# Performance work log

Measured on AMD Instinct MI355X. Metric: run time of the kernel, lower is better.

Reference implementation:

```python
import jax, jax.numpy as jnp
import numpy as np

B, S, D, H = 1, 4096, 1024, 16
HD = D // H  # head_dim = 64
NEG = -1e9


def _rotate_half(x):
    x1, x2 = jnp.split(x, 2, axis=-1)
    return jnp.concatenate([-x2, x1], axis=-1)


def _apply_rope(x, cos, sin):
    # x: [b, s, h, hd]; cos/sin: [s, hd] -> broadcast over batch and heads
    c = cos[None, :, None, :]
    s = sin[None, :, None, :]
    return x * c + _rotate_half(x) * s


def setup_inputs() -> dict:
    key = jax.random.key(0)
    kx, kq, ko = jax.random.split(key, 3)
    x = jax.random.normal(kx, (B, S, D), dtype=jnp.float32)
    # causal additive mask (finite large-negative for safe grads)
    i = jnp.arange(S)
    attn_mask = jnp.where(i[None, :] > i[:, None], NEG, 0.0).astype(jnp.float32)[None, None]
    # standard RoPE tables
    inv_freq = 1.0 / (10000.0 ** (np.arange(0, HD, 2, dtype=np.float32) / HD))
    ang = np.arange(S, dtype=np.float32)[:, None] * inv_freq[None, :]  # [S, HD/2]
    ang = np.concatenate([ang, ang], axis=-1)  # [S, HD]
    rope_cos = jnp.asarray(np.cos(ang))
    rope_sin = jnp.asarray(np.sin(ang))
    W_qkv = jax.random.normal(kq, (D, 3 * D), dtype=jnp.float32) * (D ** -0.5)
    W_out = jax.random.normal(ko, (D, D), dtype=jnp.float32) * (D ** -0.5)
    return {"x": x, "attn_mask": attn_mask, "rope_cos": rope_cos,
            "rope_sin": rope_sin, "W_qkv": W_qkv, "W_out": W_out}


def reference(x, attn_mask, rope_cos, rope_sin, W_qkv, W_out):
    b, s, d = x.shape
    qkv = x @ W_qkv                              # [b, s, 3d]
    q, k, v = jnp.split(qkv, 3, axis=-1)
    q = q.reshape(b, s, H, HD)
    k = k.reshape(b, s, H, HD)
    v = v.reshape(b, s, H, HD)
    q = _apply_rope(q, rope_cos, rope_sin)
    k = _apply_rope(k, rope_cos, rope_sin)
    att = jnp.einsum('bqhd,bkhd->bhqk', q, k) / jnp.sqrt(jnp.float32(HD))
    att = att + attn_mask                        # additive mask broadcast [b,h,s,s]
    att = jax.nn.softmax(att, axis=-1)
    out = jnp.einsum('bhqk,bkhd->bqhd', att, v).reshape(b, s, d)
    return out @ W_out
```

## Files before the change

### kernel.cpp

```cpp
#include <hip/hip_runtime.h>


typedef __attribute__((ext_vector_type(8)))  __bf16 bf16x8;
typedef __attribute__((ext_vector_type(4)))  float  f32x4;
typedef __attribute__((ext_vector_type(16))) float  f32x16;
typedef __attribute__((ext_vector_type(8)))  unsigned short ushort8;
typedef __attribute__((ext_vector_type(4)))  unsigned int   u32x4;

#define MFMA16(a,b,c) __builtin_amdgcn_mfma_f32_16x16x32_bf16((a),(b),(c),0,0,0)
#define MFMA32(a,b,c) __builtin_amdgcn_mfma_f32_32x32x16_bf16((a),(b),(c),0,0,0)

static __device__ __forceinline__ unsigned short f2bf(float f) {
  unsigned int u = __builtin_bit_cast(unsigned int, f);
  u = (u + 0x7FFFu + ((u >> 16) & 1u)) >> 16;
  return (unsigned short)u;
}
static __device__ __forceinline__ float bf2f(unsigned short u) {
  return __builtin_bit_cast(float, (unsigned int)u << 16);
}
static __device__ __forceinline__ unsigned int cvtpk(float a, float b) {
  unsigned int r;
  asm("v_cvt_pk_bf16_f32 %0, %1, %2" : "=v"(r) : "v"(a), "v"(b));
  return r;
}
static __device__ __forceinline__ void plswap(unsigned int& a, unsigned int& b) {
#if __has_builtin(__builtin_amdgcn_permlane32_swap)
  auto r = __builtin_amdgcn_permlane32_swap(a, b, false, false);
  a = r[0]; b = r[1];
#else
  unsigned int xa = (unsigned int)__shfl_xor((int)a, 32);
  unsigned int xb = (unsigned int)__shfl_xor((int)b, 32);
  int lane = __builtin_amdgcn_mbcnt_hi(~0u, __builtin_amdgcn_mbcnt_lo(~0u, 0));
  bool hi = lane >= 32;
  a = hi ? xb : a;
  b = hi ? b : xa;
#endif
}
static __device__ __forceinline__ void gll16(const unsigned short* gp, const unsigned short* lp) {
  unsigned int m0v = __builtin_amdgcn_readfirstlane((unsigned int)(unsigned long long)(uintptr_t)lp);
  asm volatile("s_mov_b32 m0, %0\n\tglobal_load_lds_dwordx4 %1, off"
               :: "s"(m0v), "v"(gp) : "memory");
}
static __device__ __forceinline__ void wait_dma() {
  asm volatile("s_waitcnt vmcnt(0)" ::: "memory");
}

__global__ __launch_bounds__(256) void prep_a(const float* __restrict__ x,
                                              const float* __restrict__ W_qkv,
                                              const float* __restrict__ W_out,
                                              unsigned short* __restrict__ xbf,
                                              unsigned short* __restrict__ WqkvT,
                                              unsigned short* __restrict__ WoutT) {
  __shared__ float t[32][33];
  int b = blockIdx.x, tid = threadIdx.x;
  if (b < 4096) {
    int i = (b * 256 + tid) * 4;
    float4 v = *reinterpret_cast<const float4*>(x + i);
    ushort4 u;
    u.x = f2bf(v.x); u.y = f2bf(v.y); u.z = f2bf(v.z); u.w = f2bf(v.w);
    *reinterpret_cast<ushort4*>(xbf + i) = u;
    return;
  }
  const float* W; unsigned short* WT; int R, C, cx, ry;
  if (b < 4096 + 3072) {
    int idx = b - 4096; W = W_qkv; WT = WqkvT; R = 1024; C = 3072;
    cx = idx % 96; ry = idx / 96;
  } else {
    int idx = b - 7168; W = W_out; WT = WoutT; R = 1024; C = 1024;
    cx = idx % 32; ry = idx / 32;
  }
  int c0 = cx * 32, r0 = ry * 32;
  int tx = tid & 31, ty = tid >> 5;
#pragma unroll
  for (int i = 0; i < 32; i += 8)
    t[ty + i][tx] = W[(size_t)(r0 + ty + i) * C + c0 + tx];
  __syncthreads();
#pragma unroll
  for (int i = 0; i < 32; i += 8)
    WT[(size_t)(c0 + ty + i) * R + r0 + tx] = f2bf(t[tx][ty + i]);
}

template <typename OutT>
__global__ __launch_bounds__(256) void gemm_lds(const unsigned short* __restrict__ A,
                                                const unsigned short* __restrict__ BT,
                                                OutT* __restrict__ C, int M, int N, int K) {
  __shared__ __align__(16) unsigned short As[128 * 32];
  __shared__ __align__(16) unsigned short Bs[128 * 32];
  int tid = threadIdx.x;
  int lane = tid & 63, w = tid >> 6;
  int wr = w >> 1, wc = w & 1;
  int row0 = blockIdx.y * 128, col0 = blockIdx.x * 128;
  int lr = lane & 15, lk = lane >> 4;
  f32x4 acc[4][4] = {};
  for (int k0 = 0; k0 < K; k0 += 32) {
#pragma unroll
    for (int i = 0; i < 2; ++i) {
      int c = i * 256 + tid;
      int r = c >> 2, cc = (c & 3) * 8;
      gll16(A  + (size_t)(row0 + r) * K + k0 + cc, &As[i * 2048 + w * 512]);
      gll16(BT + (size_t)(col0 + r) * K + k0 + cc, &Bs[i * 2048 + w * 512]);
    }
    wait_dma();
    __syncthreads();
    bf16x8 a[4], b[4];
#pragma unroll
    for (int m = 0; m < 4; m++)
      a[m] = *reinterpret_cast<const bf16x8*>(&As[(wr * 64 + m * 16 + lr) * 32 + lk * 8]);
#pragma unroll
    for (int n = 0; n < 4; n++)
      b[n] = *reinterpret_cast<const bf16x8*>(&Bs[(wc * 64 + n * 16 + lr) * 32 + lk * 8]);
#pragma unroll
    for (int m = 0; m < 4; m++)
#pragma unroll
      for (int n = 0; n < 4; n++)
        acc[m][n] = MFMA16(a[m], b[n], acc[m][n]);
    __syncthreads();
  }
#pragma unroll
  for (int m = 0; m < 4; m++)
#pragma unroll
    for (int n = 0; n < 4; n++)
#pragma unroll
      for (int r = 0; r < 4; r++) {
        size_t off = (size_t)(row0 + wr * 64 + m * 16 + lk * 4 + r) * N + col0 + wc * 64 + n * 16 + lr;
        if constexpr (sizeof(OutT) == 2) C[off] = f2bf(acc[m][n][r]);
        else                             C[off] = acc[m][n][r];
      }
}

__global__ __launch_bounds__(256) void prep_b(const unsigned short* __restrict__ qkv,
                                              const float* __restrict__ cosb,
                                              const float* __restrict__ sinb,
                                              unsigned short* __restrict__ Q,
                                              unsigned short* __restrict__ K,
                                              unsigned short* __restrict__ VF) {
  __shared__ unsigned short tile[32][68];
  int b = blockIdx.x, tid = threadIdx.x;
  if (b < 2048) {
    const float QSCALE = 0.125f * 1.4426950408889634f;
    int idx = b * 256 + tid;
    int c = idx & 7, s = (idx >> 3) & 4095, h = idx >> 15;
    int d0 = c * 8;
    int base = s * 3072 + h * 64;
    ushort8 qv  = *reinterpret_cast<const ushort8*>(qkv + base + d0);
    ushort8 qv2 = *reinterpret_cast<const ushort8*>(qkv + base + (d0 ^ 32));
    ushort8 kv  = *reinterpret_cast<const ushort8*>(qkv + base + 1024 + d0);
    ushort8 kv2 = *reinterpret_cast<const ushort8*>(qkv + base + 1024 + (d0 ^ 32));
    float sign = (d0 < 32) ? -1.f : 1.f;
    const float4* cp = reinterpret_cast<const float4*>(cosb + s * 64 + d0);
    const float4* sp = reinterpret_cast<const float4*>(sinb + s * 64 + d0);
    float4 c0 = cp[0], c1 = cp[1], s0 = sp[0], s1 = sp[1];
    float co[8] = {c0.x, c0.y, c0.z, c0.w, c1.x, c1.y, c1.z, c1.w};
    float si[8] = {s0.x, s0.y, s0.z, s0.w, s1.x, s1.y, s1.z, s1.w};
    ushort8 qo, ko;
#pragma unroll
    for (int j = 0; j < 8; ++j) {
      float q = bf2f(qv[j]), q2 = bf2f(qv2[j]);
      float k = bf2f(kv[j]), k2 = bf2f(kv2[j]);
      qo[j] = f2bf((q * co[j] + sign * q2 * si[j]) * QSCALE);
      ko[j] = f2bf(k * co[j] + sign * k2 * si[j]);
    }
    *reinterpret_cast<ushort8*>(Q + (size_t)h * 262144 + (size_t)s * 64 + d0) = qo;
    int tt = s >> 5, ql = s & 31, lo = (d0 >> 3) & 1, f = d0 >> 4;
    size_t koff = (size_t)h * 262144 + (size_t)tt * 2048 + (size_t)f * 512
                + (size_t)(lo * 32 + ql) * 8;
    *reinterpret_cast<ushort8*>(K + koff) = ko;
    return;
  }
  int vb = b - 2048;
  int t = vb & 127, h = vb >> 7;
  {
    int r = tid >> 3, c8 = (tid & 7) * 8;
    *reinterpret_cast<ushort8*>(&tile[r][c8]) =
        *reinterpret_cast<const ushort8*>(qkv + (size_t)(t * 32 + r) * 3072 + 2048 + h * 64 + c8);
  }
  __syncthreads();
  int f = tid >> 6, lane = tid & 63;
  int ql = lane & 31, lo = lane >> 5;
  int sb = (f & 1) * 16 + lo * 8;
  int d  = (f >> 1) * 32 + ql;
  ushort8 v;
#pragma unroll
  for (int j = 0; j < 8; ++j) v[j] = tile[sb + j][d];
  *reinterpret_cast<ushort8*>(VF + (size_t)h * 262144 + (size_t)t * 2048
                              + (size_t)f * 512 + (size_t)lane * 8) = v;
}

__global__ __launch_bounds__(256) void flash_attn32(const unsigned short* __restrict__ Q,
                                                    const unsigned short* __restrict__ Kf,
                                                    const unsigned short* __restrict__ Vf,
                                                    unsigned short* __restrict__ O) {
  const int S = 4096;
  __shared__ __align__(16) unsigned short sbuf[2][4][2048];
  __shared__ float lmrg[2][64];
  int flat = blockIdx.x;
  int xcd = flat & 7;
  int v = flat >> 3;
  int h2 = v >> 6, a = (v >> 5) & 1, u = v & 31;
  int h = xcd * 2 + h2;
  int base = a ? (2 * u) : (126 - 2 * u);
  int tid = threadIdx.x;
  int lane = tid & 63, w = tid >> 6;
  int qm = w & 1, pp = w >> 1;
  int ql = lane & 31, lo = lane >> 5;
  const unsigned short* Qh  = Q  + (size_t)h * S * 64;
  const unsigned short* KfH = Kf + (size_t)h * S * 64;
  const unsigned short* VfH = Vf + (size_t)h * S * 64;

  const unsigned short* img_src = (w & 1) ? VfH : KfH;
  int img_dt = w >> 1;
  auto stage = [&](int nb, int win) {
    int t = 2 * win + img_dt;
    const unsigned short* src = img_src + (size_t)t * 2048;
    const unsigned short* dst = &sbuf[nb][w][0];
#pragma unroll
    for (int j = 0; j < 4; ++j)
      gll16(src + j * 512 + lane * 8, dst + j * 512);
  };

  int qt = base + qm;
  int q0 = qt * 32;
  int nwin = base / 2 + 1;
  bf16x8 qf[4];
#pragma unroll
  for (int f = 0; f < 4; ++f)
    qf[f] = *reinterpret_cast<const bf16x8*>(Qh + (q0 + ql) * 64 + f * 16 + lo * 8);
  f32x16 oT0 = {}, oT1 = {};
  float l = 0.f;

  stage(0, 0);
  wait_dma();
  __syncthreads();
  int cb = 0;
  for (int win = 0; win < nwin; ++win) {
    if (win + 1 < nwin) stage(cb ^ 1, win + 1);
    int t = 2 * win + pp;
    if (t <= qt) {
      const unsigned short* kb = &sbuf[cb][2 * pp][0];
      const unsigned short* vb = &sbuf[cb][2 * pp + 1][0];
      bf16x8 k0 = *reinterpret_cast<const bf16x8*>(kb + 0 * 512 + lane * 8);
      bf16x8 k1 = *reinterpret_cast<const bf16x8*>(kb + 1 * 512 + lane * 8);
      bf16x8 k2 = *reinterpret_cast<const bf16x8*>(kb + 2 * 512 + lane * 8);
      bf16x8 k3 = *reinterpret_cast<const bf16x8*>(kb + 3 * 512 + lane * 8);
      f32x16 p = {};
      __builtin_amdgcn_s_setprio(1);
      p = MFMA32(k0, qf[0], p);
      p = MFMA32(k1, qf[1], p);
      p = MFMA32(k2, qf[2], p);
      p = MFMA32(k3, qf[3], p);
      __builtin_amdgcn_s_setprio(0);
      bf16x8 v00 = *reinterpret_cast<const bf16x8*>(vb + 0 * 512 + lane * 8);
      bf16x8 v01 = *reinterpret_cast<const bf16x8*>(vb + 1 * 512 + lane * 8);
      bf16x8 v10 = *reinterpret_cast<const bf16x8*>(vb + 2 * 512 + lane * 8);
      bf16x8 v11 = *reinterpret_cast<const bf16x8*>(vb + 3 * 512 + lane * 8);
      if (t == qt) {
#pragma unroll
        for (int r = 0; r < 16; ++r) {
          int kvr = (r & 3) + 8 * (r >> 2) + 4 * lo;
          if (kvr > ql) p[r] = -1e9f;
        }
      }
#pragma unroll
      for (int r = 0; r < 16; ++r) p[r] = __builtin_amdgcn_exp2f(p[r]);
      {
        float s0 = (p[0] + p[1])   + (p[2] + p[3]);
        float s1 = (p[4] + p[5])   + (p[6] + p[7]);
        float s2 = (p[8] + p[9])   + (p[10] + p[11]);
        float s3 = (p[12] + p[13]) + (p[14] + p[15]);
        l += (s0 + s1) + (s2 + s3);
      }
      unsigned int A0 = cvtpk(p[0],  p[1]),  A1 = cvtpk(p[2],  p[3]);
      unsigned int B0 = cvtpk(p[4],  p[5]),  B1 = cvtpk(p[6],  p[7]);
      plswap(A0, B0); plswap(A1, B1);
      u32x4 w0 = {A0, A1, B0, B1};
      bf16x8 P0 = __builtin_bit_cast(bf16x8, w0);
      unsigned int C0 = cvtpk(p[8],  p[9]),  C1 = cvtpk(p[10], p[11]);
      unsigned int D0 = cvtpk(p[12], p[13]), D1 = cvtpk(p[14], p[15]);
      plswap(C0, D0); plswap(C1, D1);
      u32x4 w1 = {C0, C1, D0, D1};
      bf16x8 P1 = __builtin_bit_cast(bf16x8, w1);
      __builtin_amdgcn_s_setprio(1);
      oT0 = MFMA32(v00, P0, oT0);
      oT1 = MFMA32(v10, P0, oT1);
      oT0 = MFMA32(v01, P1, oT0);
      oT1 = MFMA32(v11, P1, oT1);
      __builtin_amdgcn_s_setprio(0);
    }
    wait_dma();
    __syncthreads();
    cb ^= 1;
  }

  float* fm = reinterpret_cast<float*>(&sbuf[0][0][0]);
  if (pp == 1) {
    float* dst = fm + (qm * 64 + lane) * 33;
#pragma unroll
    for (int r = 0; r < 16; ++r) { dst[r] = oT0[r]; dst[16 + r] = oT1[r]; }
    lmrg[qm][lane] = l;
  }
  __syncthreads();
  if (pp == 0) {
    const float* src = fm + (qm * 64 + lane) * 33;
#pragma unroll
    for (int r = 0; r < 16; ++r) {
      oT0[r] += src[r];
      oT1[r] += src[16 + r];
    }
    l += lmrg[qm][lane];
    l += __shfl_xor(l, 32);
    float rl = 1.0f / l;
    size_t obase = (size_t)(q0 + ql) * 1024 + h * 64;
#pragma unroll
    for (int r = 0; r < 16; ++r) {
      int d = (r & 3) + 8 * (r >> 2) + 4 * lo;
      O[obase + d]      = f2bf(oT0[r] * rl);
      O[obase + 32 + d] = f2bf(oT1[r] * rl);
    }
  }
}

extern "C" void kernel_launch(void* const* d_in, const int* in_sizes, int n_in,
                              void* d_out, int out_size, void* d_ws, size_t ws_size,
                              hipStream_t stream) {
  const float* x        = (const float*)d_in[0];
  const float* rope_cos = (const float*)d_in[2];
  const float* rope_sin = (const float*)d_in[3];
  const float* W_qkv    = (const float*)d_in[4];
  const float* W_out    = (const float*)d_in[5];
  float* out = (float*)d_out;

  char* ws = (char*)d_ws;
  const size_t MB = 1u << 20;
  unsigned short* xbf   = (unsigned short*)(ws + 0 * MB);
  unsigned short* WqkvT = (unsigned short*)(ws + 8 * MB);
  unsigned short* WoutT = (unsigned short*)(ws + 14 * MB);
  unsigned short* qkv   = (unsigned short*)(ws + 16 * MB);
  unsigned short* Qb    = (unsigned short*)(ws + 40 * MB);
  unsigned short* Kfb   = (unsigned short*)(ws + 48 * MB);
  unsigned short* Vfb   = (unsigned short*)(ws + 56 * MB);
  unsigned short* Ob    = (unsigned short*)(ws + 64 * MB);

  prep_a<<<8192, 256, 0, stream>>>(x, W_qkv, W_out, xbf, WqkvT, WoutT);

  gemm_lds<unsigned short><<<dim3(3072 / 128, 4096 / 128), 256, 0, stream>>>(
      xbf, WqkvT, qkv, 4096, 3072, 1024);

  prep_b<<<4096, 256, 0, stream>>>(qkv, rope_cos, rope_sin, Qb, Kfb, Vfb);

  flash_attn32<<<1024, 256, 0, stream>>>(Qb, Kfb, Vfb, Ob);

  gemm_lds<float><<<dim3(1024 / 128, 4096 / 128), 256, 0, stream>>>(
      Ob, WoutT, out, 4096, 1024, 1024);
}
```

Measured before the change: 142.2 us.

## Fuse RoPE, Q scaling and Q/K layout into QKV GEMM epilogue

Adds a specialised QKV GEMM whose epilogue applies RoPE, folds the softmax scale into Q, and writes Q and K straight into the layouts the attention kernel reads. V is written to a compact buffer and reshuffled by a smaller v_frag kernel. This drops the full bf16 qkv intermediate round trip and most of the prep_b work. In exchange the epilogue does scattered 2-byte stores and per-element cos/sin loads, and the flash kernel's l-merge scratch now lives in the reused sbuf.

```diff
diff --git a/kernel.cpp b/kernel.cpp
--- a/kernel.cpp
+++ b/kernel.cpp
@@ -80,6 +80,92 @@
     WT[(size_t)(c0 + ty + i) * R + r0 + tx] = f2bf(t[tx][ty + i]);
 }
 
+__global__ __launch_bounds__(256) void gemm_qkv(const unsigned short* __restrict__ A,
+                                                const unsigned short* __restrict__ BT,
+                                                const float* __restrict__ cosb,
+                                                const float* __restrict__ sinb,
+                                                unsigned short* __restrict__ Qb,
+                                                unsigned short* __restrict__ Kf,
+                                                unsigned short* __restrict__ Vc) {
+  const int K = 1024, N = 3072;
+  __shared__ __align__(16) unsigned short As[128 * 32];
+  __shared__ __align__(16) unsigned short Bs[128 * 32];
+  int tid = threadIdx.x;
+  int lane = tid & 63, w = tid >> 6;
+  int wr = w >> 1, wc = w & 1;
+  int row0 = blockIdx.y * 128, col0 = blockIdx.x * 128;
+  int lr = lane & 15, lk = lane >> 4;
+  f32x4 acc[4][4] = {};
+  for (int k0 = 0; k0 < K; k0 += 32) {
+#pragma unroll
+    for (int i = 0; i < 2; ++i) {
+      int c = i * 256 + tid;
+      int r = c >> 2, cc = (c & 3) * 8;
+      gll16(A  + (size_t)(row0 + r) * K + k0 + cc, &As[i * 2048 + w * 512]);
+      gll16(BT + (size_t)(col0 + r) * K + k0 + cc, &Bs[i * 2048 + w * 512]);
+    }
+    wait_dma();
+    __syncthreads();
+    bf16x8 a[4], b[4];
+#pragma unroll
+    for (int m = 0; m < 4; m++)
+      a[m] = *reinterpret_cast<const bf16x8*>(&As[(wr * 64 + m * 16 + lr) * 32 + lk * 8]);
+#pragma unroll
+    for (int n = 0; n < 4; n++)
+      b[n] = *reinterpret_cast<const bf16x8*>(&Bs[(wc * 64 + n * 16 + lr) * 32 + lk * 8]);
+#pragma unroll
+    for (int m = 0; m < 4; m++)
+#pragma unroll
+      for (int n = 0; n < 4; n++)
+        acc[m][n] = MFMA16(a[m], b[n], acc[m][n]);
+    __syncthreads();
+  }
+  int colbase = col0 + wc * 64;
+  int region = colbase >> 10;
+  if (region == 2) {
+    int vc0 = colbase - 2048;
+#pragma unroll
+    for (int m = 0; m < 4; m++)
+#pragma unroll
+      for (int r = 0; r < 4; r++) {
+        int s = row0 + wr * 64 + m * 16 + lk * 4 + r;
+#pragma unroll
+        for (int n = 0; n < 4; n++)
+          Vc[(size_t)s * 1024 + vc0 + n * 16 + lr] = f2bf(acc[m][n][r]);
+      }
+  } else {
+    const float QSCALE = 0.125f * 1.4426950408889634f;
+    int h = (colbase & 1023) >> 6;
+    bool isQ = (region == 0);
+#pragma unroll
+    for (int m = 0; m < 4; m++)
+#pragma unroll
+      for (int r = 0; r < 4; r++) {
+        int s = row0 + wr * 64 + m * 16 + lk * 4 + r;
+        float c0 = cosb[s * 64 + lr],      c1 = cosb[s * 64 + 16 + lr];
+        float s0 = sinb[s * 64 + lr],      s1 = sinb[s * 64 + 16 + lr];
+        float o0 = acc[m][0][r] * c0 - acc[m][2][r] * s0;
+        float o1 = acc[m][1][r] * c1 - acc[m][3][r] * s1;
+        float o2 = acc[m][2][r] * c0 + acc[m][0][r] * s0;
+        float o3 = acc[m][3][r] * c1 + acc[m][1][r] * s1;
+        if (isQ) {
+          size_t base = (size_t)h * 262144 + (size_t)s * 64;
+          Qb[base + lr]      = f2bf(o0 * QSCALE);
+          Qb[base + 16 + lr] = f2bf(o1 * QSCALE);
+          Qb[base + 32 + lr] = f2bf(o2 * QSCALE);
+          Qb[base + 48 + lr] = f2bf(o3 * QSCALE);
+        } else {
+          size_t base = (size_t)h * 262144 + (size_t)(s >> 5) * 2048
+                      + (size_t)(((lr >> 3) & 1) * 32 + (s & 31)) * 8 + (lr & 7);
+          Kf[base]        = f2bf(o0);
+          Kf[base + 512]  = f2bf(o1);
+          Kf[base + 1024] = f2bf(o2);
+          Kf[base + 1536] = f2bf(o3);
+        }
+      }
+  }
+}
+
 template <typename OutT>
 __global__ __launch_bounds__(256) void gemm_lds(const unsigned short* __restrict__ A,
                                                 const unsigned short* __restrict__ BT,
@@ -128,51 +214,15 @@
       }
 }
 
-__global__ __launch_bounds__(256) void prep_b(const unsigned short* __restrict__ qkv,
-                                              const float* __restrict__ cosb,
-                                              const float* __restrict__ sinb,
-                                              unsigned short* __restrict__ Q,
-                                              unsigned short* __restrict__ K,
+__global__ __launch_bounds__(256) void v_frag(const unsigned short* __restrict__ Vc,
                                               unsigned short* __restrict__ VF) {
   __shared__ unsigned short tile[32][68];
   int b = blockIdx.x, tid = threadIdx.x;
-  if (b < 2048) {
-    const float QSCALE = 0.125f * 1.4426950408889634f;
-    int idx = b * 256 + tid;
-    int c = idx & 7, s = (idx >> 3) & 4095, h = idx >> 15;
-    int d0 = c * 8;
-    int base = s * 3072 + h * 64;
-    ushort8 qv  = *reinterpret_cast<const ushort8*>(qkv + base + d0);
-    ushort8 qv2 = *reinterpret_cast<const ushort8*>(qkv + base + (d0 ^ 32));
-    ushort8 kv  = *reinterpret_cast<const ushort8*>(qkv + base + 1024 + d0);
-    ushort8 kv2 = *reinterpret_cast<const ushort8*>(qkv + base + 1024 + (d0 ^ 32));
-    float sign = (d0 < 32) ? -1.f : 1.f;
-    const float4* cp = reinterpret_cast<const float4*>(cosb + s * 64 + d0);
-    const float4* sp = reinterpret_cast<const float4*>(sinb + s * 64 + d0);
-    float4 c0 = cp[0], c1 = cp[1], s0 = sp[0], s1 = sp[1];
-    float co[8] = {c0.x, c0.y, c0.z, c0.w, c1.x, c1.y, c1.z, c1.w};
-    float si[8] = {s0.x, s0.y, s0.z, s0.w, s1.x, s1.y, s1.z, s1.w};
-    ushort8 qo, ko;
-#pragma unroll
-    for (int j = 0; j < 8; ++j) {
-      float q = bf2f(qv[j]), q2 = bf2f(qv2[j]);
-      float k = bf2f(kv[j]), k2 = bf2f(kv2[j]);
-      qo[j] = f2bf((q * co[j] + sign * q2 * si[j]) * QSCALE);
-      ko[j] = f2bf(k * co[j] + sign * k2 * si[j]);
-    }
-    *reinterpret_cast<ushort8*>(Q + (size_t)h * 262144 + (size_t)s * 64 + d0) = qo;
-    int tt = s >> 5, ql = s & 31, lo = (d0 >> 3) & 1, f = d0 >> 4;
-    size_t koff = (size_t)h * 262144 + (size_t)tt * 2048 + (size_t)f * 512
-                + (size_t)(lo * 32 + ql) * 8;
-    *reinterpret_cast<ushort8*>(K + koff) = ko;
-    return;
-  }
-  int vb = b - 2048;
-  int t = vb & 127, h = vb >> 7;
+  int t = b & 127, h = b >> 7;
   {
     int r = tid >> 3, c8 = (tid & 7) * 8;
     *reinterpret_cast<ushort8*>(&tile[r][c8]) =
-        *reinterpret_cast<const ushort8*>(qkv + (size_t)(t * 32 + r) * 3072 + 2048 + h * 64 + c8);
+        *reinterpret_cast<const ushort8*>(Vc + (size_t)(t * 32 + r) * 1024 + h * 64 + c8);
   }
   __syncthreads();
   int f = tid >> 6, lane = tid & 63;
@@ -192,7 +242,6 @@
                                                     unsigned short* __restrict__ O) {
   const int S = 4096;
   __shared__ __align__(16) unsigned short sbuf[2][4][2048];
-  __shared__ float lmrg[2][64];
   int flat = blockIdx.x;
   int xcd = flat & 7;
   int v = flat >> 3;
@@ -292,11 +341,12 @@
   }
 
   float* fm = reinterpret_cast<float*>(&sbuf[0][0][0]);
+  float* lm = fm + 2 * 64 * 33;
   if (pp == 1) {
     float* dst = fm + (qm * 64 + lane) * 33;
 #pragma unroll
     for (int r = 0; r < 16; ++r) { dst[r] = oT0[r]; dst[16 + r] = oT1[r]; }
-    lmrg[qm][lane] = l;
+    lm[qm * 64 + lane] = l;
   }
   __syncthreads();
   if (pp == 0) {
@@ -306,7 +356,7 @@
       oT0[r] += src[r];
       oT1[r] += src[16 + r];
     }
-    l += lmrg[qm][lane];
+    l += lm[qm * 64 + lane];
     l += __shfl_xor(l, 32);
     float rl = 1.0f / l;
     size_t obase = (size_t)(q0 + ql) * 1024 + h * 64;
@@ -334,18 +384,18 @@
   unsigned short* xbf   = (unsigned short*)(ws + 0 * MB);
   unsigned short* WqkvT = (unsigned short*)(ws + 8 * MB);
   unsigned short* WoutT = (unsigned short*)(ws + 14 * MB);
-  unsigned short* qkv   = (unsigned short*)(ws + 16 * MB);
-  unsigned short* Qb    = (unsigned short*)(ws + 40 * MB);
-  unsigned short* Kfb   = (unsigned short*)(ws + 48 * MB);
-  unsigned short* Vfb   = (unsigned short*)(ws + 56 * MB);
-  unsigned short* Ob    = (unsigned short*)(ws + 64 * MB);
+  unsigned short* Qb    = (unsigned short*)(ws + 16 * MB);
+  unsigned short* Kfb   = (unsigned short*)(ws + 24 * MB);
+  unsigned short* Vc    = (unsigned short*)(ws + 32 * MB);
+  unsigned short* Vfb   = (unsigned short*)(ws + 40 * MB);
+  unsigned short* Ob    = (unsigned short*)(ws + 48 * MB);
 
   prep_a<<<8192, 256, 0, stream>>>(x, W_qkv, W_out, xbf, WqkvT, WoutT);
 
-  gemm_lds<unsigned short><<<dim3(3072 / 128, 4096 / 128), 256, 0, stream>>>(
-      xbf, WqkvT, qkv, 4096, 3072, 1024);
-
-  prep_b<<<4096, 256, 0, stream>>>(qkv, rope_cos, rope_sin, Qb, Kfb, Vfb);
+  gemm_qkv<<<dim3(3072 / 128, 4096 / 128), 256, 0, stream>>>(
+      xbf, WqkvT, rope_cos, rope_sin, Qb, Kfb, Vc);
+
+  v_frag<<<2048, 256, 0, stream>>>(Vc, Vfb);
 
   flash_attn32<<<1024, 256, 0, stream>>>(Qb, Kfb, Vfb, Ob);
 
```

Result: slower. 153.6 us (+8.1%).
